# Kernel optimization log

Measured on AMD Instinct MI355X. Metric: run time of the kernel, lower is better.

Reference implementation:

```python
import jax, jax.numpy as jnp
import numpy as np

# DAG configuration (fixed, mirrors the networkx dG used at construction time)
B = 4096          # batch
N_INP = 4096      # genes
L0 = 512          # leaf GO terms, each mapped to G disjoint genes
G = 8             # genes per leaf term
H = 16            # module_neurons (uniform per-module hidden size)
FAN = 8           # children per internal module -> input size FAN*H = 128
L1, L2 = 64, 8    # internal level sizes; root has L2=8 children


def setup_inputs() -> dict:
    key = jax.random.key(0)
    ks = jax.random.split(key, 8)
    s = lambda *sh: 0.1
    x = jax.random.normal(ks[0], (B, N_INP), dtype=jnp.float32)
    # Gene (RestrictedLayer) effective weights: kernel*connections is one-hot,
    # so only kernel[gene_idx[m,j], j] survives -> store as [L0, G] + bias.
    Wg = jax.random.normal(ks[1], (L0, G), dtype=jnp.float32) * 0.1
    bg = jax.random.normal(ks[2], (L0, G), dtype=jnp.float32) * 0.1
    # Per-level module Dense kernels (sigmoid, no bias)
    W0 = jax.random.normal(ks[3], (L0, G, H), dtype=jnp.float32) * 0.1       # leaf terms: G -> H
    W1 = jax.random.normal(ks[4], (L1, FAN * H, H), dtype=jnp.float32) * 0.1  # 128 -> 16
    W2 = jax.random.normal(ks[5], (L2, FAN * H, H), dtype=jnp.float32) * 0.1  # 128 -> 16
    W3 = jax.random.normal(ks[6], (FAN * H, H), dtype=jnp.float32) * 0.1      # root: 128 -> 16
    Wf = jax.random.normal(ks[7], (H, 1), dtype=jnp.float32) * 0.1            # final linear, no bias
    return {"x": x, "Wg": Wg, "bg": bg, "W0": W0, "W1": W1, "W2": W2,
            "W3": W3, "Wf": Wf}


def reference(x, Wg, bg, W0, W1, W2, W3, Wf):
    b = x.shape[0]
    # Input gene layers (RestrictedLayer, linear activation):
    # leaf m owns contiguous genes [m*G, (m+1)*G) -> gather is a reshape.
    gene_out = x.reshape(b, L0, G) * Wg + bg                    # [B, L0, G]
    # Level 0 (leaf GO terms): Dense(G->H), sigmoid, no bias
    h0 = jax.nn.sigmoid(jnp.einsum('bmg,mgh->bmh', gene_out, W0))   # [B, L0, H]
    # Level 1: concat FAN children's H outputs -> Dense(FAN*H -> H), sigmoid
    h1 = jax.nn.sigmoid(jnp.einsum('bmk,mkh->bmh',
                                   h0.reshape(b, L1, FAN * H), W1))  # [B, L1, H]
    # Level 2
    h2 = jax.nn.sigmoid(jnp.einsum('bmk,mkh->bmh',
                                   h1.reshape(b, L2, FAN * H), W2))  # [B, L2, H]
    # Root 'GO:output'
    hr = jax.nn.sigmoid(h2.reshape(b, FAN * H) @ W3)                 # [B, H]
    # Final Dense(1), linear, no bias
    return hr @ Wf                                                   # [B, 1]
```

## Files before the change

### kernel.cpp

```cpp
#include <hip/hip_runtime.h>
#include <hip/hip_bf16.h>


#define TB 8
#define H0S 1032
#define H1S 136

typedef __attribute__((ext_vector_type(8))) short short8;
typedef __attribute__((ext_vector_type(4))) float floatx4;
typedef __attribute__((address_space(3))) void lds_void;
typedef const __attribute__((address_space(1))) void gbl_void;

__device__ __forceinline__ float sigf(float v) {
    return __builtin_amdgcn_rcpf(1.0f + __expf(-v));
}
__device__ __forceinline__ unsigned int f2bf_u32(float f) {
    unsigned int u = __builtin_bit_cast(unsigned int, f);
    return (u + 0x7fffu + ((u >> 16) & 1u)) >> 16;
}
__device__ __forceinline__ unsigned short f2bf(float f) {
    return (unsigned short)f2bf_u32(f);
}
__device__ __forceinline__ unsigned int f2bf2(float lo, float hi) {
    return f2bf_u32(lo) | (f2bf_u32(hi) << 16);
}

__global__ __launch_bounds__(256) void k_prep(
    const float* __restrict__ W1, const float* __restrict__ W2,
    unsigned short* __restrict__ W1t, unsigned short* __restrict__ W2t)
{
    __shared__ float wl[128 * 17];
    const int mb = blockIdx.x;
    const float* src = (mb < 64) ? (W1 + (size_t)mb * 2048)
                                 : (W2 + (size_t)(mb - 64) * 2048);
    unsigned short* dst = (mb < 64) ? (W1t + (size_t)mb * 2048)
                                    : (W2t + (size_t)(mb - 64) * 2048);
    const int tid = threadIdx.x;
#pragma unroll
    for (int i = 0; i < 8; ++i) {
        const int idx = tid + i * 256;
        wl[(idx >> 4) * 17 + (idx & 15)] = src[idx];
    }
    __syncthreads();
#pragma unroll
    for (int i = 0; i < 4; ++i) {
        const int u  = tid + i * 256;
        const int h  = u >> 6;
        const int k  = (u & 63) * 2;
        ((unsigned int*)dst)[u] = f2bf2(wl[k * 17 + h], wl[(k + 1) * 17 + h]);
    }
}

__global__ __launch_bounds__(256) void k_tree(
    const float* __restrict__ x, const float* __restrict__ Wg,
    const float* __restrict__ bg, const float* __restrict__ W0,
    const unsigned short* __restrict__ W1t, const unsigned short* __restrict__ W2t,
    float* __restrict__ h2ws)
{
    __shared__ __align__(16) float xs[TB * 512];
    __shared__ __align__(16) unsigned short h0s[TB * H0S];
    __shared__ __align__(16) unsigned short h1s[TB * H1S];

    const int tid  = threadIdx.x;
    const int s    = blockIdx.x & 7;
    const int b0   = (blockIdx.x >> 3) * TB;
    const int lane = tid & 63;
    const int wv   = tid >> 6;
    const int m_l  = tid >> 2;
    const int hq   = tid & 3;
    const int m    = s * 64 + m_l;

    {
        const float* xbase = x + (size_t)b0 * 4096 + s * 512;
#pragma unroll
        for (int t = 0; t < 4; ++t) {
            const int i    = (t * 4 + wv) * 64 + lane;
            const int row  = i >> 7;
            const int colf = (i & 127) * 4;
            gbl_void* gp = (gbl_void*)(xbase + (size_t)row * 4096 + colf);
            lds_void* lp = (lds_void*)((char*)xs + (size_t)(t * 4 + wv) * 1024);
            __builtin_amdgcn_global_load_lds(gp, lp, 16, 0, 0);
        }
    }

    float4 w0r[8];
#pragma unroll
    for (int g = 0; g < 8; ++g)
        w0r[g] = *(const float4*)(W0 + (size_t)m * 128 + g * 16 + hq * 4);
    const float4 wg0 = *(const float4*)(Wg + m * 8);
    const float4 wg1 = *(const float4*)(Wg + m * 8 + 4);
    const float4 bg0 = *(const float4*)(bg + m * 8);
    const float4 bg1 = *(const float4*)(bg + m * 8 + 4);
    __syncthreads();

    {
        const float* xb = &xs[m_l * 8];
        unsigned short* h0base = &h0s[m_l * 16 + hq * 4];
#pragma unroll
        for (int b = 0; b < TB; ++b) {
            const float4 xv0 = *(const float4*)(xb + b * 512);
            const float4 xv1 = *(const float4*)(xb + b * 512 + 4);
            float gene[8];
            gene[0] = fmaf(xv0.x, wg0.x, bg0.x);
            gene[1] = fmaf(xv0.y, wg0.y, bg0.y);
            gene[2] = fmaf(xv0.z, wg0.z, bg0.z);
            gene[3] = fmaf(xv0.w, wg0.w, bg0.w);
            gene[4] = fmaf(xv1.x, wg1.x, bg1.x);
            gene[5] = fmaf(xv1.y, wg1.y, bg1.y);
            gene[6] = fmaf(xv1.z, wg1.z, bg1.z);
            gene[7] = fmaf(xv1.w, wg1.w, bg1.w);
            float a0 = 0.f, a1 = 0.f, a2 = 0.f, a3 = 0.f;
#pragma unroll
            for (int g = 0; g < 8; ++g) {
                a0 = fmaf(gene[g], w0r[g].x, a0);
                a1 = fmaf(gene[g], w0r[g].y, a1);
                a2 = fmaf(gene[g], w0r[g].z, a2);
                a3 = fmaf(gene[g], w0r[g].w, a3);
            }
            *(uint2*)(h0base + b * H0S) =
                make_uint2(f2bf2(sigf(a0), sigf(a1)), f2bf2(sigf(a2), sigf(a3)));
        }
    }
    __syncthreads();

    const int n = lane & 15, q = lane >> 4;
    {
#pragma unroll
        for (int jj = 0; jj < 2; ++jj) {
            const int j = wv * 2 + jj;
            const unsigned short* w1m =
                W1t + ((size_t)(s * 8 + j) * 16 + n) * 128 + q * 8;
            const unsigned short* am = &h0s[(n & 7) * H0S + j * 128 + q * 8];
            floatx4 acc = {0.f, 0.f, 0.f, 0.f};
#pragma unroll
            for (int ks = 0; ks < 4; ++ks) {
                const short8 av = *(const short8*)(am + ks * 32);
                const short8 bv = *(const short8*)(w1m + ks * 32);
                acc = __builtin_amdgcn_mfma_f32_16x16x32_bf16(av, bv, acc, 0, 0, 0);
            }
            if (q < 2) {
#pragma unroll
                for (int r = 0; r < 4; ++r)
                    h1s[(q * 4 + r) * H1S + j * 16 + n] = f2bf(sigf(acc[r]));
            }
        }
    }
    __syncthreads();

    if (wv == 0) {
        const unsigned short* w2m = W2t + ((size_t)s * 16 + n) * 128 + q * 8;
        const unsigned short* am = &h1s[(n & 7) * H1S + q * 8];
        floatx4 acc = {0.f, 0.f, 0.f, 0.f};
#pragma unroll
        for (int ks = 0; ks < 4; ++ks) {
            const short8 av = *(const short8*)(am + ks * 32);
            const short8 bv = *(const short8*)(w2m + ks * 32);
            acc = __builtin_amdgcn_mfma_f32_16x16x32_bf16(av, bv, acc, 0, 0, 0);
        }
        if (q < 2) {
#pragma unroll
            for (int r = 0; r < 4; ++r)
                h2ws[(size_t)(b0 + q * 4 + r) * 128 + s * 16 + n] = sigf(acc[r]);
        }
    }
}

__global__ __launch_bounds__(128) void k_root(
    const float* __restrict__ h2ws, const float* __restrict__ W3,
    const float* __restrict__ Wf, float* __restrict__ out)
{
    __shared__ float w3s[2048];
    __shared__ float wfs[16];
    const int tid = threadIdx.x;
#pragma unroll
    for (int t = 0; t < 16; ++t) w3s[tid + t * 128] = W3[tid + t * 128];
    if (tid < 16) wfs[tid] = Wf[tid];
    __syncthreads();

    const int h = tid & 15;
    const int b = blockIdx.x * 8 + (tid >> 4);
    const float4* hp = (const float4*)(h2ws + (size_t)b * 128);
    float acc = 0.f;
#pragma unroll
    for (int k4 = 0; k4 < 32; ++k4) {
        const float4 hv = hp[k4];
        acc = fmaf(hv.x, w3s[(k4 * 4 + 0) * 16 + h], acc);
        acc = fmaf(hv.y, w3s[(k4 * 4 + 1) * 16 + h], acc);
        acc = fmaf(hv.z, w3s[(k4 * 4 + 2) * 16 + h], acc);
        acc = fmaf(hv.w, w3s[(k4 * 4 + 3) * 16 + h], acc);
    }
    float v = sigf(acc) * wfs[h];
    v += __shfl_down(v, 8, 16);
    v += __shfl_down(v, 4, 16);
    v += __shfl_down(v, 2, 16);
    v += __shfl_down(v, 1, 16);
    if (h == 0) out[b] = v;
}

extern "C" void kernel_launch(void* const* d_in, const int* in_sizes, int n_in,
                              void* d_out, int out_size, void* d_ws, size_t ws_size,
                              hipStream_t stream) {
    const float* x  = (const float*)d_in[0];
    const float* Wg = (const float*)d_in[1];
    const float* bg = (const float*)d_in[2];
    const float* W0 = (const float*)d_in[3];
    const float* W1 = (const float*)d_in[4];
    const float* W2 = (const float*)d_in[5];
    const float* W3 = (const float*)d_in[6];
    const float* Wf = (const float*)d_in[7];
    float* out = (float*)d_out;

    float* h2 = (float*)d_ws;
    unsigned short* W1t = (unsigned short*)((char*)d_ws + (size_t)2 * 1024 * 1024);
    unsigned short* W2t = W1t + (size_t)64 * 2048;

    k_prep<<<dim3(72), dim3(256), 0, stream>>>(W1, W2, W1t, W2t);
    k_tree<<<dim3((4096 / TB) * 8), dim3(256), 0, stream>>>(x, Wg, bg, W0, W1t, W2t, h2);
    k_root<<<dim3(4096 / 8), dim3(128), 0, stream>>>(h2, W3, Wf, out);
}
```

Before: 125.9 us.

## Fold gene layer into W0, halve batch tile, preload W1/W2 fragments

```diff
diff --git a/kernel.cpp b/kernel.cpp
--- a/kernel.cpp
+++ b/kernel.cpp
@@ -2,7 +2,7 @@
 #include <hip/hip_bf16.h>
 
 
-#define TB 8
+#define TB 4
 #define H0S 1032
 #define H1S 136
 
@@ -27,33 +27,49 @@
 
 __global__ __launch_bounds__(256) void k_prep(
     const float* __restrict__ W1, const float* __restrict__ W2,
-    unsigned short* __restrict__ W1t, unsigned short* __restrict__ W2t)
+    const float* __restrict__ W0, const float* __restrict__ Wg,
+    const float* __restrict__ bg,
+    unsigned short* __restrict__ W1t, unsigned short* __restrict__ W2t,
+    float* __restrict__ W0g, float* __restrict__ bias0)
 {
     __shared__ float wl[128 * 17];
     const int mb = blockIdx.x;
-    const float* src = (mb < 64) ? (W1 + (size_t)mb * 2048)
-                                 : (W2 + (size_t)(mb - 64) * 2048);
-    unsigned short* dst = (mb < 64) ? (W1t + (size_t)mb * 2048)
-                                    : (W2t + (size_t)(mb - 64) * 2048);
     const int tid = threadIdx.x;
-#pragma unroll
-    for (int i = 0; i < 8; ++i) {
-        const int idx = tid + i * 256;
-        wl[(idx >> 4) * 17 + (idx & 15)] = src[idx];
-    }
-    __syncthreads();
-#pragma unroll
-    for (int i = 0; i < 4; ++i) {
-        const int u  = tid + i * 256;
-        const int h  = u >> 6;
-        const int k  = (u & 63) * 2;
-        ((unsigned int*)dst)[u] = f2bf2(wl[k * 17 + h], wl[(k + 1) * 17 + h]);
+    if (mb < 72) {
+        const float* src = (mb < 64) ? (W1 + (size_t)mb * 2048)
+                                     : (W2 + (size_t)(mb - 64) * 2048);
+        unsigned short* dst = (mb < 64) ? (W1t + (size_t)mb * 2048)
+                                        : (W2t + (size_t)(mb - 64) * 2048);
+#pragma unroll
+        for (int i = 0; i < 8; ++i) {
+            const int idx = tid + i * 256;
+            wl[(idx >> 4) * 17 + (idx & 15)] = src[idx];
+        }
+        __syncthreads();
+#pragma unroll
+        for (int i = 0; i < 4; ++i) {
+            const int u = tid + i * 256;
+            const int h = u >> 6;
+            const int k = (u & 63) * 2;
+            ((unsigned int*)dst)[u] = f2bf2(wl[k * 17 + h], wl[(k + 1) * 17 + h]);
+        }
+    } else {
+        const int m = (mb - 72) * 16 + (tid >> 4);
+        const int h = tid & 15;
+        float bias = 0.f;
+#pragma unroll
+        for (int g = 0; g < 8; ++g) {
+            const float w0 = W0[(size_t)m * 128 + g * 16 + h];
+            W0g[((size_t)m * 16 + h) * 8 + g] = Wg[m * 8 + g] * w0;
+            bias = fmaf(bg[m * 8 + g], w0, bias);
+        }
+        bias0[m * 16 + h] = bias;
     }
 }
 
 __global__ __launch_bounds__(256) void k_tree(
-    const float* __restrict__ x, const float* __restrict__ Wg,
-    const float* __restrict__ bg, const float* __restrict__ W0,
+    const float* __restrict__ x, const float* __restrict__ W0g,
+    const float* __restrict__ bias0,
     const unsigned short* __restrict__ W1t, const unsigned short* __restrict__ W2t,
     float* __restrict__ h2ws)
 {
@@ -66,14 +82,11 @@
     const int b0   = (blockIdx.x >> 3) * TB;
     const int lane = tid & 63;
     const int wv   = tid >> 6;
-    const int m_l  = tid >> 2;
-    const int hq   = tid & 3;
-    const int m    = s * 64 + m_l;
 
     {
         const float* xbase = x + (size_t)b0 * 4096 + s * 512;
 #pragma unroll
-        for (int t = 0; t < 4; ++t) {
+        for (int t = 0; t < 2; ++t) {
             const int i    = (t * 4 + wv) * 64 + lane;
             const int row  = i >> 7;
             const int colf = (i & 127) * 4;
@@ -83,14 +96,25 @@
         }
     }
 
-    float4 w0r[8];
-#pragma unroll
-    for (int g = 0; g < 8; ++g)
-        w0r[g] = *(const float4*)(W0 + (size_t)m * 128 + g * 16 + hq * 4);
-    const float4 wg0 = *(const float4*)(Wg + m * 8);
-    const float4 wg1 = *(const float4*)(Wg + m * 8 + 4);
-    const float4 bg0 = *(const float4*)(bg + m * 8);
-    const float4 bg1 = *(const float4*)(bg + m * 8 + 4);
+    const int m_l = tid >> 2;
+    const int hq  = tid & 3;
+    const int m   = s * 64 + m_l;
+    float4 wA[4][2];
+#pragma unroll
+    for (int hi = 0; hi < 4; ++hi) {
+        wA[hi][0] = *(const float4*)(W0g + ((size_t)m * 16 + hq * 4 + hi) * 8);
+        wA[hi][1] = *(const float4*)(W0g + ((size_t)m * 16 + hq * 4 + hi) * 8 + 4);
+    }
+    const float4 bv = *(const float4*)(bias0 + m * 16 + hq * 4);
+    const float bb[4] = {bv.x, bv.y, bv.z, bv.w};
+
+    const int n = lane & 15, q = lane >> 4;
+    short8 w1r0[4];
+    {
+        const unsigned short* w1m = W1t + ((size_t)(s * 8 + wv * 2) * 16 + n) * 128 + q * 8;
+#pragma unroll
+        for (int ks = 0; ks < 4; ++ks) w1r0[ks] = *(const short8*)(w1m + ks * 32);
+    }
     __syncthreads();
 
     {
@@ -98,69 +122,78 @@
         unsigned short* h0base = &h0s[m_l * 16 + hq * 4];
 #pragma unroll
         for (int b = 0; b < TB; ++b) {
-            const float4 xv0 = *(const float4*)(xb + b * 512);
-            const float4 xv1 = *(const float4*)(xb + b * 512 + 4);
-            float gene[8];
-            gene[0] = fmaf(xv0.x, wg0.x, bg0.x);
-            gene[1] = fmaf(xv0.y, wg0.y, bg0.y);
-            gene[2] = fmaf(xv0.z, wg0.z, bg0.z);
-            gene[3] = fmaf(xv0.w, wg0.w, bg0.w);
-            gene[4] = fmaf(xv1.x, wg1.x, bg1.x);
-            gene[5] = fmaf(xv1.y, wg1.y, bg1.y);
-            gene[6] = fmaf(xv1.z, wg1.z, bg1.z);
-            gene[7] = fmaf(xv1.w, wg1.w, bg1.w);
-            float a0 = 0.f, a1 = 0.f, a2 = 0.f, a3 = 0.f;
-#pragma unroll
-            for (int g = 0; g < 8; ++g) {
-                a0 = fmaf(gene[g], w0r[g].x, a0);
-                a1 = fmaf(gene[g], w0r[g].y, a1);
-                a2 = fmaf(gene[g], w0r[g].z, a2);
-                a3 = fmaf(gene[g], w0r[g].w, a3);
+            const float4 x0 = *(const float4*)(xb + b * 512);
+            const float4 x1 = *(const float4*)(xb + b * 512 + 4);
+            float a[4];
+#pragma unroll
+            for (int hi = 0; hi < 4; ++hi) {
+                float v = bb[hi];
+                v = fmaf(x0.x, wA[hi][0].x, v);
+                v = fmaf(x0.y, wA[hi][0].y, v);
+                v = fmaf(x0.z, wA[hi][0].z, v);
+                v = fmaf(x0.w, wA[hi][0].w, v);
+                v = fmaf(x1.x, wA[hi][1].x, v);
+                v = fmaf(x1.y, wA[hi][1].y, v);
+                v = fmaf(x1.z, wA[hi][1].z, v);
+                v = fmaf(x1.w, wA[hi][1].w, v);
+                a[hi] = v;
             }
             *(uint2*)(h0base + b * H0S) =
-                make_uint2(f2bf2(sigf(a0), sigf(a1)), f2bf2(sigf(a2), sigf(a3)));
-        }
-    }
-    __syncthreads();
-
-    const int n = lane & 15, q = lane >> 4;
-    {
-#pragma unroll
-        for (int jj = 0; jj < 2; ++jj) {
-            const int j = wv * 2 + jj;
-            const unsigned short* w1m =
-                W1t + ((size_t)(s * 8 + j) * 16 + n) * 128 + q * 8;
-            const unsigned short* am = &h0s[(n & 7) * H0S + j * 128 + q * 8];
-            floatx4 acc = {0.f, 0.f, 0.f, 0.f};
-#pragma unroll
-            for (int ks = 0; ks < 4; ++ks) {
-                const short8 av = *(const short8*)(am + ks * 32);
-                const short8 bv = *(const short8*)(w1m + ks * 32);
-                acc = __builtin_amdgcn_mfma_f32_16x16x32_bf16(av, bv, acc, 0, 0, 0);
-            }
-            if (q < 2) {
-#pragma unroll
-                for (int r = 0; r < 4; ++r)
-                    h1s[(q * 4 + r) * H1S + j * 16 + n] = f2bf(sigf(acc[r]));
-            }
+                make_uint2(f2bf2(sigf(a[0]), sigf(a[1])), f2bf2(sigf(a[2]), sigf(a[3])));
+        }
+    }
+    __syncthreads();
+
+    {
+        const int j0 = wv * 2;
+        short8 w1r1[4];
+        const unsigned short* w1m1 = W1t + ((size_t)(s * 8 + j0 + 1) * 16 + n) * 128 + q * 8;
+#pragma unroll
+        for (int ks = 0; ks < 4; ++ks) w1r1[ks] = *(const short8*)(w1m1 + ks * 32);
+
+        const unsigned short* am0 = &h0s[(n & 3) * H0S + j0 * 128 + q * 8];
+        floatx4 acc0 = {0.f, 0.f, 0.f, 0.f};
+#pragma unroll
+        for (int ks = 0; ks < 4; ++ks) {
+            const short8 av = *(const short8*)(am0 + ks * 32);
+            acc0 = __builtin_amdgcn_mfma_f32_16x16x32_bf16(av, w1r0[ks], acc0, 0, 0, 0);
+        }
+        if (q == 0) {
+#pragma unroll
+            for (int r = 0; r < 4; ++r)
+                h1s[r * H1S + j0 * 16 + n] = f2bf(sigf(acc0[r]));
+        }
+        const unsigned short* am1 = am0 + 128;
+        floatx4 acc1 = {0.f, 0.f, 0.f, 0.f};
+#pragma unroll
+        for (int ks = 0; ks < 4; ++ks) {
+            const short8 av = *(const short8*)(am1 + ks * 32);
+            acc1 = __builtin_amdgcn_mfma_f32_16x16x32_bf16(av, w1r1[ks], acc1, 0, 0, 0);
+        }
+        if (q == 0) {
+#pragma unroll
+            for (int r = 0; r < 4; ++r)
+                h1s[r * H1S + (j0 + 1) * 16 + n] = f2bf(sigf(acc1[r]));
         }
     }
     __syncthreads();
 
     if (wv == 0) {
+        short8 w2r[4];
         const unsigned short* w2m = W2t + ((size_t)s * 16 + n) * 128 + q * 8;
-        const unsigned short* am = &h1s[(n & 7) * H1S + q * 8];
+#pragma unroll
+        for (int ks = 0; ks < 4; ++ks) w2r[ks] = *(const short8*)(w2m + ks * 32);
+        const unsigned short* am = &h1s[(n & 3) * H1S + q * 8];
         floatx4 acc = {0.f, 0.f, 0.f, 0.f};
 #pragma unroll
         for (int ks = 0; ks < 4; ++ks) {
             const short8 av = *(const short8*)(am + ks * 32);
-            const short8 bv = *(const short8*)(w2m + ks * 32);
-            acc = __builtin_amdgcn_mfma_f32_16x16x32_bf16(av, bv, acc, 0, 0, 0);
-        }
-        if (q < 2) {
+            acc = __builtin_amdgcn_mfma_f32_16x16x32_bf16(av, w2r[ks], acc, 0, 0, 0);
+        }
+        if (q == 0) {
 #pragma unroll
             for (int r = 0; r < 4; ++r)
-                h2ws[(size_t)(b0 + q * 4 + r) * 128 + s * 16 + n] = sigf(acc[r]);
+                h2ws[(size_t)(b0 + r) * 128 + s * 16 + n] = sigf(acc[r]);
         }
     }
 }
@@ -210,11 +243,14 @@
     const float* Wf = (const float*)d_in[7];
     float* out = (float*)d_out;
 
-    float* h2 = (float*)d_ws;
-    unsigned short* W1t = (unsigned short*)((char*)d_ws + (size_t)2 * 1024 * 1024);
-    unsigned short* W2t = W1t + (size_t)64 * 2048;
-
-    k_prep<<<dim3(72), dim3(256), 0, stream>>>(W1, W2, W1t, W2t);
-    k_tree<<<dim3((4096 / TB) * 8), dim3(256), 0, stream>>>(x, Wg, bg, W0, W1t, W2t, h2);
+    char* ws = (char*)d_ws;
+    float* h2            = (float*)ws;
+    unsigned short* W1t  = (unsigned short*)(ws + (2u << 20));
+    unsigned short* W2t  = (unsigned short*)(ws + (2u << 20) + (256u << 10));
+    float* W0g           = (float*)(ws + (2u << 20) + (512u << 10));
+    float* bias0         = (float*)(ws + (2u << 20) + (768u << 10));
+
+    k_prep<<<dim3(104), dim3(256), 0, stream>>>(W1, W2, W0, Wg, bg, W1t, W2t, W0g, bias0);
+    k_tree<<<dim3((4096 / TB) * 8), dim3(256), 0, stream>>>(x, W0g, bias0, W1t, W2t, h2);
     k_root<<<dim3(4096 / 8), dim3(128), 0, stream>>>(h2, W3, Wf, out);
 }
```

New measurement: 162.4 us. +29.0%, slower.
